# Performance work log

Hardware: AMD Instinct MI355X
Metric: run time of the kernel (lower is better)

Reference implementation:

```python
import jax, jax.numpy as jnp
import numpy as np

SEQ, BATCH, N_IN, N_HID, N_CLS = 128, 16384, 28, 100, 10


def setup_inputs() -> dict:
    key = jax.random.key(0)
    ks = jax.random.split(key, 7)
    s_in = 1.0 / np.sqrt(N_IN)
    s_h = 1.0 / np.sqrt(N_HID)
    return {
        "data": jax.random.normal(ks[0], (SEQ, BATCH, N_IN), dtype=jnp.float32),
        "w_xh": jax.random.uniform(ks[1], (N_IN, N_HID), jnp.float32, -s_in, s_in),
        "b_xh": jax.random.uniform(ks[2], (N_HID,), jnp.float32, -s_in, s_in),
        "w_hh": jax.random.uniform(ks[3], (N_HID, N_HID), jnp.float32, -s_h, s_h),
        "b_hh": jax.random.uniform(ks[4], (N_HID,), jnp.float32, -s_h, s_h),
        "w_fc": jax.random.uniform(ks[5], (N_HID, N_CLS), jnp.float32, -s_h, s_h),
        "b_fc": jax.random.uniform(ks[6], (N_CLS,), jnp.float32, -s_h, s_h),
    }


def reference(data, w_xh, b_xh, w_hh, b_hh, w_fc, b_fc):
    # Precompute input projections for all timesteps in one big GEMM:
    # [T, B, n_in] @ [n_in, H] -> [T, B, H]
    xh = jnp.einsum("tbi,ih->tbh", data, w_xh) + b_xh + b_hh

    def step(h, xh_t):
        h = jnp.tanh(xh_t + h @ w_hh)
        return h, None

    h0 = jnp.zeros((data.shape[1], w_hh.shape[0]), dtype=data.dtype)
    h_T, _ = jax.lax.scan(step, h0, xh)
    return h_T @ w_fc + b_fc  # [B, cls]
```

## Files before the change

### kernel.cpp

```cpp
#include <hip/hip_runtime.h>


#define SEQ   128
#define BATCH 16384
#define NIN   28
#define NHID  100
#define NCLS  10

#define HSTR  136
#define WROWS 112

typedef __bf16 bf16x8 __attribute__((ext_vector_type(8)));
typedef float  f32x4  __attribute__((ext_vector_type(4)));

__device__ __forceinline__ unsigned short f2bf(float f) {
    unsigned u = __builtin_bit_cast(unsigned, f);
    u += 0x7FFFu + ((u >> 16) & 1u);
    return (unsigned short)(u >> 16);
}
__device__ __forceinline__ float bf2f(unsigned short b) {
    unsigned u = ((unsigned)b) << 16;
    return __builtin_bit_cast(float, u);
}
__device__ __forceinline__ float tanh_fast(float x) {
    float t = __expf(2.0f * x);
    float r = __builtin_amdgcn_rcpf(t + 1.0f);
    return __builtin_fmaf(-2.0f, r, 1.0f);
}
__device__ __forceinline__ unsigned cvt_pk_bf16(float lo, float hi) {
    unsigned d;
    asm("v_cvt_pk_bf16_f32 %0, %1, %2" : "=v"(d) : "v"(lo), "v"(hi));
    return d;
}

__global__ __launch_bounds__(256, 4) void rnn_fused_kernel(
    const float* __restrict__ data, const float* __restrict__ w_xh,
    const float* __restrict__ b_xh, const float* __restrict__ w_hh,
    const float* __restrict__ b_hh, const float* __restrict__ w_fc,
    const float* __restrict__ b_fc, float* __restrict__ out)
{
    __shared__ unsigned short pool[WROWS * HSTR];
    unsigned short* WT = pool;
    unsigned short* hb = pool;

    const int tid  = threadIdx.x;
    const int wid  = tid >> 6;
    const int lane = tid & 63;
    const int x    = lane & 15;
    const int g    = lane >> 4;
    const int m0   = blockIdx.x * 16;

    const int JT0 = wid * 2;
    const int NT  = (wid < 3) ? 2 : 1;

    for (int idx = tid; idx < WROWS * HSTR; idx += 256) {
        int j = idx % WROWS;
        int k = idx / WROWS;
        float v = 0.0f;
        if (j < NHID) {
            if (k < NHID)            v = w_hh[k * NHID + j];
            else if (k < NHID + NIN) v = w_xh[(k - NHID) * NHID + j];
        }
        WT[j * HSTR + k] = f2bf(v);
    }
    __syncthreads();

    bf16x8 aw[2][4];
    #pragma unroll
    for (int jl = 0; jl < 2; ++jl)
        if (jl < NT)
            #pragma unroll
            for (int kt = 0; kt < 4; ++kt)
                aw[jl][kt] = *(const bf16x8*)&WT[((JT0 + jl) * 16 + x) * HSTR + kt * 32 + g * 8];

    f32x4 biasf[2];
    #pragma unroll
    for (int jl = 0; jl < 2; ++jl)
        #pragma unroll
        for (int r = 0; r < 4; ++r) {
            int j  = (JT0 + jl) * 16 + g * 4 + r;
            int jc = (j < NHID) ? j : (NHID - 1);
            biasf[jl][r] = b_xh[jc] + b_hh[jc];
        }
    __syncthreads();

    {
        unsigned int* hb32 = (unsigned int*)hb;
        for (int idx = tid; idx < (16 * HSTR) / 2; idx += 256) hb32[idx] = 0u;
    }
    __syncthreads();
    if (tid < 224) {
        float2 v = *(const float2*)(data + (size_t)m0 * NIN + 2 * tid);
        int m = tid / 14, i2 = 2 * (tid - m * 14);
        *(unsigned int*)&hb[m * HSTR + NHID + i2] = cvt_pk_bf16(v.x, v.y);
    }
    __syncthreads();

    for (int t = 0; t < SEQ; ++t) {
        unsigned short* cur = hb + (t & 1) * (16 * HSTR);
        unsigned short* nxt = hb + ((t & 1) ^ 1) * (16 * HSTR);

        float2 xv[4];
        if (wid == 3) {
            int t1 = (t < SEQ - 1) ? t + 1 : t;
            const float* src = data + ((size_t)t1 * BATCH + m0) * NIN;
            #pragma unroll
            for (int r = 0; r < 4; ++r) {
                int idx = r * 64 + lane;
                if (idx < 224) xv[r] = *(const float2*)(src + 2 * idx);
            }
        }

        bf16x8 bq[4];
        #pragma unroll
        for (int kt = 0; kt < 4; ++kt)
            bq[kt] = *(const bf16x8*)&cur[x * HSTR + kt * 32 + g * 8];

        f32x4 acc[2];
        acc[0] = biasf[0];
        acc[1] = biasf[1];
        #pragma unroll
        for (int kt = 0; kt < 4; ++kt) {
            acc[0] = __builtin_amdgcn_mfma_f32_16x16x32_bf16(aw[0][kt], bq[kt], acc[0], 0, 0, 0);
            if (NT > 1)
                acc[1] = __builtin_amdgcn_mfma_f32_16x16x32_bf16(aw[1][kt], bq[kt], acc[1], 0, 0, 0);
        }

        #pragma unroll
        for (int jl = 0; jl < 2; ++jl) {
            if (jl < NT) {
                int j0 = (JT0 + jl) * 16 + 4 * g;
                float t0 = tanh_fast(acc[jl][0]);
                float t1 = tanh_fast(acc[jl][1]);
                float t2 = tanh_fast(acc[jl][2]);
                float t3 = tanh_fast(acc[jl][3]);
                if (j0 < NHID) {
                    unsigned lo = cvt_pk_bf16(t0, t1);
                    unsigned hi = cvt_pk_bf16(t2, t3);
                    unsigned long long q = ((unsigned long long)hi << 32) | (unsigned long long)lo;
                    *(unsigned long long*)&nxt[x * HSTR + j0] = q;
                }
            }
        }
        if (wid == 3) {
            #pragma unroll
            for (int r = 0; r < 4; ++r) {
                int idx = r * 64 + lane;
                if (idx < 224) {
                    int m = idx / 14, i2 = 2 * (idx - m * 14);
                    *(unsigned int*)&nxt[m * HSTR + NHID + i2] = cvt_pk_bf16(xv[r].x, xv[r].y);
                }
            }
        }
        __syncthreads();
    }

    for (int o = tid; o < 16 * NCLS; o += 256) {
        int m = o / NCLS, c = o - (o / NCLS) * NCLS;
        float s = b_fc[c];
        for (int j = 0; j < NHID; ++j)
            s = __builtin_fmaf(bf2f(hb[m * HSTR + j]), w_fc[j * NCLS + c], s);
        out[(size_t)(m0 + m) * NCLS + c] = s;
    }
}

extern "C" void kernel_launch(void* const* d_in, const int* in_sizes, int n_in,
                              void* d_out, int out_size, void* d_ws, size_t ws_size,
                              hipStream_t stream) {
    const float* data = (const float*)d_in[0];
    const float* w_xh = (const float*)d_in[1];
    const float* b_xh = (const float*)d_in[2];
    const float* w_hh = (const float*)d_in[3];
    const float* b_hh = (const float*)d_in[4];
    const float* w_fc = (const float*)d_in[5];
    const float* b_fc = (const float*)d_in[6];
    float* outp = (float*)d_out;
    (void)in_sizes; (void)n_in; (void)out_size; (void)d_ws; (void)ws_size;
    rnn_fused_kernel<<<dim3(BATCH / 16), dim3(256), 0, stream>>>(
        data, w_xh, b_xh, w_hh, b_hh, w_fc, b_fc, outp);
}
```

Measured before the change: 383.0 us.

## Split work into seven MFMA warps plus a dedicated input-loader warp

Raises the block from 4 to 8 wavefronts. Seven waves each compute one 16-row output tile with a single MFMA chain, and the eighth wave only prefetches and converts the next timestep's input into shared memory. This shortens each wave's serial MFMA and tanh chain per step and separates input loading from compute. In exchange it doubles the threads that take part in every per-step barrier and lowers the number of blocks that can sit on each CU.

```diff
diff --git a/kernel.cpp b/kernel.cpp
--- a/kernel.cpp
+++ b/kernel.cpp
@@ -33,7 +33,7 @@
     return d;
 }
 
-__global__ __launch_bounds__(256, 4) void rnn_fused_kernel(
+__global__ __launch_bounds__(512, 8) void rnn_fused_kernel(
     const float* __restrict__ data, const float* __restrict__ w_xh,
     const float* __restrict__ b_xh, const float* __restrict__ w_hh,
     const float* __restrict__ b_hh, const float* __restrict__ w_fc,
@@ -50,10 +50,9 @@
     const int g    = lane >> 4;
     const int m0   = blockIdx.x * 16;
 
-    const int JT0 = wid * 2;
-    const int NT  = (wid < 3) ? 2 : 1;
+    const bool compute = (wid < 7);
 
-    for (int idx = tid; idx < WROWS * HSTR; idx += 256) {
+    for (int idx = tid; idx < WROWS * HSTR; idx += 512) {
         int j = idx % WROWS;
         int k = idx / WROWS;
         float v = 0.0f;
@@ -65,28 +64,24 @@
     }
     __syncthreads();
 
-    bf16x8 aw[2][4];
-    #pragma unroll
-    for (int jl = 0; jl < 2; ++jl)
-        if (jl < NT)
-            #pragma unroll
-            for (int kt = 0; kt < 4; ++kt)
-                aw[jl][kt] = *(const bf16x8*)&WT[((JT0 + jl) * 16 + x) * HSTR + kt * 32 + g * 8];
-
-    f32x4 biasf[2];
-    #pragma unroll
-    for (int jl = 0; jl < 2; ++jl)
+    bf16x8 aw[4];
+    f32x4  biasf = {0.f, 0.f, 0.f, 0.f};
+    if (compute) {
+        #pragma unroll
+        for (int kt = 0; kt < 4; ++kt)
+            aw[kt] = *(const bf16x8*)&WT[(wid * 16 + x) * HSTR + kt * 32 + g * 8];
         #pragma unroll
         for (int r = 0; r < 4; ++r) {
-            int j  = (JT0 + jl) * 16 + g * 4 + r;
+            int j  = wid * 16 + g * 4 + r;
             int jc = (j < NHID) ? j : (NHID - 1);
-            biasf[jl][r] = b_xh[jc] + b_hh[jc];
+            biasf[r] = b_xh[jc] + b_hh[jc];
         }
+    }
     __syncthreads();
 
     {
         unsigned int* hb32 = (unsigned int*)hb;
-        for (int idx = tid; idx < (16 * HSTR) / 2; idx += 256) hb32[idx] = 0u;
+        for (int idx = tid; idx < (16 * HSTR) / 2; idx += 512) hb32[idx] = 0u;
     }
     __syncthreads();
     if (tid < 224) {
@@ -100,49 +95,37 @@
         unsigned short* cur = hb + (t & 1) * (16 * HSTR);
         unsigned short* nxt = hb + ((t & 1) ^ 1) * (16 * HSTR);
 
-        float2 xv[4];
-        if (wid == 3) {
-            int t1 = (t < SEQ - 1) ? t + 1 : t;
-            const float* src = data + ((size_t)t1 * BATCH + m0) * NIN;
+        if (compute) {
+            bf16x8 bq[4];
+            #pragma unroll
+            for (int kt = 0; kt < 4; ++kt)
+                bq[kt] = *(const bf16x8*)&cur[x * HSTR + kt * 32 + g * 8];
+
+            f32x4 acc = biasf;
+            #pragma unroll
+            for (int kt = 0; kt < 4; ++kt)
+                acc = __builtin_amdgcn_mfma_f32_16x16x32_bf16(aw[kt], bq[kt], acc, 0, 0, 0);
+
+            float t0 = tanh_fast(acc[0]);
+            float t1 = tanh_fast(acc[1]);
+            float t2 = tanh_fast(acc[2]);
+            float t3 = tanh_fast(acc[3]);
+            int j0 = wid * 16 + 4 * g;
+            if (j0 < NHID) {
+                unsigned lo = cvt_pk_bf16(t0, t1);
+                unsigned hi = cvt_pk_bf16(t2, t3);
+                unsigned long long q = ((unsigned long long)hi << 32) | (unsigned long long)lo;
+                *(unsigned long long*)&nxt[x * HSTR + j0] = q;
+            }
+        } else {
+            int t1s = (t < SEQ - 1) ? t + 1 : t;
+            const float* src = data + ((size_t)t1s * BATCH + m0) * NIN;
+            float2 xv[4];
             #pragma unroll
             for (int r = 0; r < 4; ++r) {
                 int idx = r * 64 + lane;
                 if (idx < 224) xv[r] = *(const float2*)(src + 2 * idx);
             }
-        }
-
-        bf16x8 bq[4];
-        #pragma unroll
-        for (int kt = 0; kt < 4; ++kt)
-            bq[kt] = *(const bf16x8*)&cur[x * HSTR + kt * 32 + g * 8];
-
-        f32x4 acc[2];
-        acc[0] = biasf[0];
-        acc[1] = biasf[1];
-        #pragma unroll
-        for (int kt = 0; kt < 4; ++kt) {
-            acc[0] = __builtin_amdgcn_mfma_f32_16x16x32_bf16(aw[0][kt], bq[kt], acc[0], 0, 0, 0);
-            if (NT > 1)
-                acc[1] = __builtin_amdgcn_mfma_f32_16x16x32_bf16(aw[1][kt], bq[kt], acc[1], 0, 0, 0);
-        }
-
-        #pragma unroll
-        for (int jl = 0; jl < 2; ++jl) {
-            if (jl < NT) {
-                int j0 = (JT0 + jl) * 16 + 4 * g;
-                float t0 = tanh_fast(acc[jl][0]);
-                float t1 = tanh_fast(acc[jl][1]);
-                float t2 = tanh_fast(acc[jl][2]);
-                float t3 = tanh_fast(acc[jl][3]);
-                if (j0 < NHID) {
-                    unsigned lo = cvt_pk_bf16(t0, t1);
-                    unsigned hi = cvt_pk_bf16(t2, t3);
-                    unsigned long long q = ((unsigned long long)hi << 32) | (unsigned long long)lo;
-                    *(unsigned long long*)&nxt[x * HSTR + j0] = q;
-                }
-            }
-        }
-        if (wid == 3) {
             #pragma unroll
             for (int r = 0; r < 4; ++r) {
                 int idx = r * 64 + lane;
@@ -155,7 +138,7 @@
         __syncthreads();
     }
 
-    for (int o = tid; o < 16 * NCLS; o += 256) {
+    for (int o = tid; o < 16 * NCLS; o += 512) {
         int m = o / NCLS, c = o - (o / NCLS) * NCLS;
         float s = b_fc[c];
         for (int j = 0; j < NHID; ++j)
@@ -176,6 +159,6 @@
     const float* b_fc = (const float*)d_in[6];
     float* outp = (float*)d_out;
     (void)in_sizes; (void)n_in; (void)out_size; (void)d_ws; (void)ws_size;
-    rnn_fused_kernel<<<dim3(BATCH / 16), dim3(256), 0, stream>>>(
+    rnn_fused_kernel<<<dim3(BATCH / 16), dim3(512), 0, stream>>>(
         data, w_xh, b_xh, w_hh, b_hh, w_fc, b_fc, outp);
 }
```

Measured after the change: 376.8 us. Within noise of the previous version (-1.6%).
